# Kernel optimization log

Measured on AMD Instinct MI355X. Metric: run time of the kernel, lower is better.

Reference implementation:

```python
import jax, jax.numpy as jnp
import numpy as np

NEG_INF = -9e15
ALPHA = 0.2  # LeakyReLU negative slope


def setup_inputs() -> dict:
    key = jax.random.key(0)
    k1, k2, k3, k4 = jax.random.split(key, 4)
    N, F_in, F_out = 8192, 128, 64
    h = jax.random.normal(k1, (N, F_in), dtype=jnp.float32)
    adj = jax.random.randint(k2, (N, N), 0, 2, dtype=jnp.int32)
    W = jax.random.normal(k3, (F_in, F_out), dtype=jnp.float32) * (1.414 / np.sqrt(F_in))
    a = jax.random.normal(k4, (2 * F_out, 1), dtype=jnp.float32) * 0.1
    return {"h": h, "adj": adj, "W": W, "a": a}


def reference(h, adj, W, a):
    # Wh: [N, F_out]
    Wh = h @ W
    F_out = Wh.shape[1]
    # Decomposed additive score: cat([Wh_i, Wh_j]) @ a == Wh_i@a1 + Wh_j@a2.
    # Identical math to the original repeat/cat/mm, without the [N*N, 2F] blowup.
    s1 = Wh @ a[:F_out, 0]   # [N] source-side score
    s2 = Wh @ a[F_out:, 0]   # [N] target-side score
    e = jax.nn.leaky_relu(s1[:, None] + s2[None, :], negative_slope=ALPHA)  # [N, N]
    attention = jax.nn.softmax(jnp.where(adj > 0, e, NEG_INF), axis=1)
    # dropout is identity in eval mode
    h_prime = attention @ Wh  # [N, F_out]
    return (h_prime, attention)
```

## Files before the change

### kernel.cpp

```cpp
#include <hip/hip_runtime.h>

#define NN 8192
#define FIN 128
#define FOUT 64
#define NEGINF (-9e15f)
#define LALPHA 0.2f

typedef float f32x4 __attribute__((ext_vector_type(4)));
typedef short short8 __attribute__((ext_vector_type(8)));

__device__ __forceinline__ unsigned short f32_to_bf16(float x) {
  unsigned int u = __float_as_uint(x);
  u = (u + 0x7fffu + ((u >> 16) & 1u)) >> 16;
  return (unsigned short)u;
}
__device__ __forceinline__ float bf16_to_f32(unsigned short b) {
  return __uint_as_float(((unsigned int)b) << 16);
}

__global__ __launch_bounds__(256) void gat_prep(
    const float* __restrict__ h, const float* __restrict__ W,
    const float* __restrict__ a,
    float* __restrict__ s1g, float* __restrict__ s2g,
    unsigned short* __restrict__ whfh)
{
  __shared__ __align__(16) float Wl[FIN * FOUT];
  __shared__ __align__(16) float hl[16 * FIN];
  const int tid = threadIdx.x;
  const int i0 = blockIdx.x * 16;
  #pragma unroll
  for (int it = 0; it < 8; ++it) {
    int idx = (it * 256 + tid) * 4;
    *(f32x4*)&Wl[idx] = *(const f32x4*)&W[idx];
  }
  #pragma unroll
  for (int it = 0; it < 2; ++it) {
    int idx = (it * 256 + tid) * 4;
    *(f32x4*)&hl[idx] = *(const f32x4*)&h[(size_t)i0 * FIN + idx];
  }
  __syncthreads();
  const int r = tid >> 4;
  const int f0 = (tid & 15) * 4;
  f32x4 acc = {0.f, 0.f, 0.f, 0.f};
  #pragma unroll 8
  for (int k = 0; k < FIN; ++k) {
    float hv = hl[r * FIN + k];
    f32x4 wv = *(const f32x4*)&Wl[k * FOUT + f0];
    acc += hv * wv;
  }
  f32x4 a1v = *(const f32x4*)&a[f0];
  f32x4 a2v = *(const f32x4*)&a[FOUT + f0];
  float p1 = acc.x * a1v.x + acc.y * a1v.y + acc.z * a1v.z + acc.w * a1v.w;
  float p2 = acc.x * a2v.x + acc.y * a2v.y + acc.z * a2v.z + acc.w * a2v.w;
  #pragma unroll
  for (int d = 1; d < 16; d <<= 1) {
    p1 += __shfl_xor(p1, d, 16);
    p2 += __shfl_xor(p2, d, 16);
  }
  const int j = i0 + r;
  if ((tid & 15) == 0) { s1g[j] = p1; s2g[j] = p2; }
  const int kstep = j >> 5;
  const int lhi = (j >> 3) & 3;
  const int ein = j & 7;
  #pragma unroll
  for (int e = 0; e < 4; ++e) {
    int f = f0 + e;
    unsigned short hb = f32_to_bf16(acc[e]);
    int ln = lhi * 16 + (f & 15);
    whfh[(size_t)(kstep * 4 + (f >> 4)) * 512 + ln * 8 + ein] = hb;
  }
}

__global__ __launch_bounds__(256, 2) void gat_main(
    const int* __restrict__ adj,
    const float* __restrict__ s1g, const float* __restrict__ s2g,
    const unsigned short* __restrict__ whfh,
    float* __restrict__ outh, float* __restrict__ outa)
{
  __shared__ __align__(16) float s2l[NN];
  __shared__ __align__(16) unsigned int maskl[16][257];
  __shared__ float rowp[16][4];
  const int tid = threadIdx.x;
  const int lane = tid & 63;
  const int wv = tid >> 6;
  const int i0 = blockIdx.x * 16;

  #pragma unroll
  for (int it = 0; it < 8; ++it) {
    int idx = (it * 256 + tid) * 4;
    *(f32x4*)&s2l[idx] = *(const f32x4*)&s2g[idx];
  }
  __syncthreads();

  {
    const int rbase = wv * 4;
    const int* __restrict__ ar0 = adj + (size_t)(i0 + rbase + 0) * NN;
    const int* __restrict__ ar1 = adj + (size_t)(i0 + rbase + 1) * NN;
    const int* __restrict__ ar2 = adj + (size_t)(i0 + rbase + 2) * NN;
    const int* __restrict__ ar3 = adj + (size_t)(i0 + rbase + 3) * NN;
    float mx0 = -3.4e38f, mx1 = -3.4e38f, mx2 = -3.4e38f, mx3 = -3.4e38f;
    #pragma unroll 2
    for (int it = 0; it < 128; ++it) {
      int jj = it * 64 + lane;
      float sv = s2l[jj];
      int a0 = __builtin_nontemporal_load(&ar0[jj]);
      int a1 = __builtin_nontemporal_load(&ar1[jj]);
      int a2 = __builtin_nontemporal_load(&ar2[jj]);
      int a3 = __builtin_nontemporal_load(&ar3[jj]);
      unsigned long long b0 = __ballot(a0 > 0);
      unsigned long long b1 = __ballot(a1 > 0);
      unsigned long long b2 = __ballot(a2 > 0);
      unsigned long long b3 = __ballot(a3 > 0);
      mx0 = fmaxf(mx0, (a0 > 0) ? sv : -3.4e38f);
      mx1 = fmaxf(mx1, (a1 > 0) ? sv : -3.4e38f);
      mx2 = fmaxf(mx2, (a2 > 0) ? sv : -3.4e38f);
      mx3 = fmaxf(mx3, (a3 > 0) ? sv : -3.4e38f);
      if ((lane & 31) == 0) {
        int hi = lane >> 5;
        maskl[rbase + 0][it * 2 + hi] = (unsigned int)(b0 >> (hi * 32));
        maskl[rbase + 1][it * 2 + hi] = (unsigned int)(b1 >> (hi * 32));
        maskl[rbase + 2][it * 2 + hi] = (unsigned int)(b2 >> (hi * 32));
        maskl[rbase + 3][it * 2 + hi] = (unsigned int)(b3 >> (hi * 32));
      }
    }
    float mxs[4] = {mx0, mx1, mx2, mx3};
    #pragma unroll
    for (int rr = 0; rr < 4; ++rr) {
      float ms = mxs[rr];
      #pragma unroll
      for (int d = 1; d < 64; d <<= 1) ms = fmaxf(ms, __shfl_xor(ms, d));
      float s1v = s1g[i0 + rbase + rr];
      float z = s1v + ms;
      float m = (ms <= -3.3e38f) ? NEGINF : (z >= 0.f ? z : LALPHA * z);
      float ls = 0.f;
      for (int it = 0; it < 128; ++it) {
        int jj = it * 64 + lane;
        unsigned int wrd = maskl[rbase + rr][it * 2 + (lane >> 5)];
        float x = s1v + s2l[jj];
        x = (x >= 0.f) ? x : LALPHA * x;
        x = ((wrd >> (lane & 31)) & 1u) ? x : NEGINF;
        ls += __expf(x - m);
      }
      #pragma unroll
      for (int d = 1; d < 64; d <<= 1) ls += __shfl_xor(ls, d);
      if (lane == 0) {
        rowp[rbase + rr][0] = s1v;
        rowp[rbase + rr][1] = m;
        rowp[rbase + rr][2] = 1.f / ls;
      }
    }
  }
  __syncthreads();

  const int row = lane & 15;
  const int kg = lane >> 4;
  const float s1r = rowp[row][0];
  const float mr = rowp[row][1];
  const float rir = rowp[row][2];
  const int kbase = wv * 2048;
  f32x4 acc0 = {0,0,0,0}, acc1 = {0,0,0,0}, acc2 = {0,0,0,0}, acc3 = {0,0,0,0};
  float* __restrict__ orow = outa + (size_t)(i0 + row) * NN;
  const short8* __restrict__ bfrag = (const short8*)whfh;
  for (int step = 0; step < 64; ++step) {
    const int k0 = kbase + step * 32;
    const int jb = k0 + kg * 8;
    f32x4 sa = *(const f32x4*)&s2l[jb];
    f32x4 sb = *(const f32x4*)&s2l[jb + 4];
    unsigned int bits = maskl[row][k0 >> 5] >> (kg * 8);
    float s2v[8] = {sa.x, sa.y, sa.z, sa.w, sb.x, sb.y, sb.z, sb.w};
    float af[8];
    short8 AH, AL;
    #pragma unroll
    for (int e = 0; e < 8; ++e) {
      float x = s1r + s2v[e];
      x = (x >= 0.f) ? x : LALPHA * x;
      x = ((bits >> e) & 1u) ? x : NEGINF;
      float p = __expf(x - mr) * rir;
      af[e] = p;
      unsigned short hb = f32_to_bf16(p);
      AH[e] = (short)hb;
      AL[e] = (short)f32_to_bf16(p - bf16_to_f32(hb));
    }
    f32x4 st0 = {af[0], af[1], af[2], af[3]};
    f32x4 st1 = {af[4], af[5], af[6], af[7]};
    __builtin_nontemporal_store(st0, (f32x4*)&orow[jb]);
    __builtin_nontemporal_store(st1, (f32x4*)&orow[jb + 4]);
    size_t fb = (size_t)(k0 >> 5) * 256 + lane;
    short8 B0 = bfrag[fb];
    short8 B1 = bfrag[fb + 64];
    short8 B2 = bfrag[fb + 128];
    short8 B3 = bfrag[fb + 192];
    acc0 = __builtin_amdgcn_mfma_f32_16x16x32_bf16(AH, B0, acc0, 0, 0, 0);
    acc1 = __builtin_amdgcn_mfma_f32_16x16x32_bf16(AH, B1, acc1, 0, 0, 0);
    acc2 = __builtin_amdgcn_mfma_f32_16x16x32_bf16(AH, B2, acc2, 0, 0, 0);
    acc3 = __builtin_amdgcn_mfma_f32_16x16x32_bf16(AH, B3, acc3, 0, 0, 0);
    acc0 = __builtin_amdgcn_mfma_f32_16x16x32_bf16(AL, B0, acc0, 0, 0, 0);
    acc1 = __builtin_amdgcn_mfma_f32_16x16x32_bf16(AL, B1, acc1, 0, 0, 0);
    acc2 = __builtin_amdgcn_mfma_f32_16x16x32_bf16(AL, B2, acc2, 0, 0, 0);
    acc3 = __builtin_amdgcn_mfma_f32_16x16x32_bf16(AL, B3, acc3, 0, 0, 0);
  }
  __syncthreads();
  float* red = (float*)&maskl[0][0];
  {
    const int c15 = lane & 15;
    f32x4 av[4] = {acc0, acc1, acc2, acc3};
    #pragma unroll
    for (int nt = 0; nt < 4; ++nt) {
      #pragma unroll
      for (int rg = 0; rg < 4; ++rg) {
        red[wv * 1024 + (kg * 4 + rg) * 64 + nt * 16 + c15] = av[nt][rg];
      }
    }
  }
  __syncthreads();
  {
    int base = tid * 4;
    f32x4 r0 = *(f32x4*)&red[base];
    f32x4 r1 = *(f32x4*)&red[1024 + base];
    f32x4 r2 = *(f32x4*)&red[2048 + base];
    f32x4 r3 = *(f32x4*)&red[3072 + base];
    f32x4 s = r0 + r1 + r2 + r3;
    *(f32x4*)&outh[(size_t)i0 * FOUT + base] = s;
  }
}

extern "C" void kernel_launch(void* const* d_in, const int* in_sizes, int n_in,
                              void* d_out, int out_size, void* d_ws, size_t ws_size,
                              hipStream_t stream) {
  const float* h = (const float*)d_in[0];
  const int* adj = (const int*)d_in[1];
  const float* W = (const float*)d_in[2];
  const float* a = (const float*)d_in[3];
  float* outh = (float*)d_out;
  float* outa = outh + (size_t)NN * FOUT;
  char* ws = (char*)d_ws;
  float* s1g = (float*)ws;
  float* s2g = s1g + NN;
  unsigned short* whfh = (unsigned short*)(ws + 64 * 1024);
  gat_prep<<<512, 256, 0, stream>>>(h, W, a, s1g, s2g, whfh);
  gat_main<<<512, 256, 0, stream>>>(adj, s1g, s2g, whfh, outh, outa);
}
```

Measured before the change: 528.4 us.

## Split mask/softmax-stats pass into separate kernel and widen attention blocks

Moves the adjacency scan, row max and row sum into a new kernel that handles one row per wave across 2048 blocks. It stashes the bitmask in the first 1KB of each output attention row, and the attention kernel reloads it from there before overwriting. The attention/MFMA kernel now uses 512 threads (8 waves) with a two-stage LDS reduction. The aim is more parallelism in the adj-reading phase and higher occupancy in the compute phase, at the cost of an extra launch and a global round trip for the mask and stats.

```diff
diff --git a/kernel.cpp b/kernel.cpp
--- a/kernel.cpp
+++ b/kernel.cpp
@@ -7,6 +7,7 @@
 #define LALPHA 0.2f
 
 typedef float f32x4 __attribute__((ext_vector_type(4)));
+typedef float f32x2 __attribute__((ext_vector_type(2)));
 typedef short short8 __attribute__((ext_vector_type(8)));
 
 __device__ __forceinline__ unsigned short f32_to_bf16(float x) {
@@ -71,84 +72,86 @@
   }
 }
 
-__global__ __launch_bounds__(256, 2) void gat_main(
+__global__ __launch_bounds__(256, 4) void gat_mask(
     const int* __restrict__ adj,
     const float* __restrict__ s1g, const float* __restrict__ s2g,
+    float* __restrict__ outa,
+    float* __restrict__ mrow, float* __restrict__ rlrow)
+{
+  __shared__ __align__(16) float s2l[NN];
+  __shared__ unsigned long long mw[4][128];
+  const int tid = threadIdx.x;
+  const int lane = tid & 63;
+  const int wv = tid >> 6;
+  const int row = blockIdx.x * 4 + wv;
+  #pragma unroll
+  for (int it = 0; it < 8; ++it) {
+    int idx = (it * 256 + tid) * 4;
+    *(f32x4*)&s2l[idx] = *(const f32x4*)&s2g[idx];
+  }
+  __syncthreads();
+  const int* __restrict__ ar = adj + (size_t)row * NN;
+  float mx = -3.4e38f;
+  #pragma unroll 4
+  for (int it = 0; it < 128; ++it) {
+    int jj = it * 64 + lane;
+    int av = __builtin_nontemporal_load(&ar[jj]);
+    unsigned long long b = __ballot(av > 0);
+    mx = fmaxf(mx, (av > 0) ? s2l[jj] : -3.4e38f);
+    if (lane == 0) mw[wv][it] = b;
+  }
+  #pragma unroll
+  for (int d = 1; d < 64; d <<= 1) mx = fmaxf(mx, __shfl_xor(mx, d));
+  const float s1v = s1g[row];
+  const float z = s1v + mx;
+  const float m = (mx <= -3.3e38f) ? NEGINF : fmaxf(z, LALPHA * z);
+  float ls = 0.f;
+  for (int it = 0; it < 128; ++it) {
+    int jj = it * 64 + lane;
+    unsigned long long b = mw[wv][it];
+    float x = s1v + s2l[jj];
+    x = fmaxf(x, LALPHA * x);
+    x = ((b >> lane) & 1ull) ? x : NEGINF;
+    ls += __expf(x - m);
+  }
+  #pragma unroll
+  for (int d = 1; d < 64; d <<= 1) ls += __shfl_xor(ls, d);
+  if (lane == 0) { mrow[row] = m; rlrow[row] = 1.f / ls; }
+  unsigned long long* mrowg = (unsigned long long*)(outa + (size_t)row * NN);
+  mrowg[lane] = mw[wv][lane];
+  mrowg[lane + 64] = mw[wv][lane + 64];
+}
+
+__global__ __launch_bounds__(512, 4) void gat_attn(
+    const float* __restrict__ s1g, const float* __restrict__ s2g,
+    const float* __restrict__ mrow, const float* __restrict__ rlrow,
     const unsigned short* __restrict__ whfh,
     float* __restrict__ outh, float* __restrict__ outa)
 {
   __shared__ __align__(16) float s2l[NN];
-  __shared__ __align__(16) unsigned int maskl[16][257];
-  __shared__ float rowp[16][4];
+  __shared__ unsigned int maskl[16][258];
+  __shared__ __align__(16) float red[4][1024];
+  __shared__ float rowp[16][3];
   const int tid = threadIdx.x;
   const int lane = tid & 63;
   const int wv = tid >> 6;
   const int i0 = blockIdx.x * 16;
 
   #pragma unroll
-  for (int it = 0; it < 8; ++it) {
-    int idx = (it * 256 + tid) * 4;
+  for (int it = 0; it < 4; ++it) {
+    int idx = (it * 512 + tid) * 4;
     *(f32x4*)&s2l[idx] = *(const f32x4*)&s2g[idx];
   }
-  __syncthreads();
-
-  {
-    const int rbase = wv * 4;
-    const int* __restrict__ ar0 = adj + (size_t)(i0 + rbase + 0) * NN;
-    const int* __restrict__ ar1 = adj + (size_t)(i0 + rbase + 1) * NN;
-    const int* __restrict__ ar2 = adj + (size_t)(i0 + rbase + 2) * NN;
-    const int* __restrict__ ar3 = adj + (size_t)(i0 + rbase + 3) * NN;
-    float mx0 = -3.4e38f, mx1 = -3.4e38f, mx2 = -3.4e38f, mx3 = -3.4e38f;
-    #pragma unroll 2
-    for (int it = 0; it < 128; ++it) {
-      int jj = it * 64 + lane;
-      float sv = s2l[jj];
-      int a0 = __builtin_nontemporal_load(&ar0[jj]);
-      int a1 = __builtin_nontemporal_load(&ar1[jj]);
-      int a2 = __builtin_nontemporal_load(&ar2[jj]);
-      int a3 = __builtin_nontemporal_load(&ar3[jj]);
-      unsigned long long b0 = __ballot(a0 > 0);
-      unsigned long long b1 = __ballot(a1 > 0);
-      unsigned long long b2 = __ballot(a2 > 0);
-      unsigned long long b3 = __ballot(a3 > 0);
-      mx0 = fmaxf(mx0, (a0 > 0) ? sv : -3.4e38f);
-      mx1 = fmaxf(mx1, (a1 > 0) ? sv : -3.4e38f);
-      mx2 = fmaxf(mx2, (a2 > 0) ? sv : -3.4e38f);
-      mx3 = fmaxf(mx3, (a3 > 0) ? sv : -3.4e38f);
-      if ((lane & 31) == 0) {
-        int hi = lane >> 5;
-        maskl[rbase + 0][it * 2 + hi] = (unsigned int)(b0 >> (hi * 32));
-        maskl[rbase + 1][it * 2 + hi] = (unsigned int)(b1 >> (hi * 32));
-        maskl[rbase + 2][it * 2 + hi] = (unsigned int)(b2 >> (hi * 32));
-        maskl[rbase + 3][it * 2 + hi] = (unsigned int)(b3 >> (hi * 32));
-      }
-    }
-    float mxs[4] = {mx0, mx1, mx2, mx3};
-    #pragma unroll
-    for (int rr = 0; rr < 4; ++rr) {
-      float ms = mxs[rr];
-      #pragma unroll
-      for (int d = 1; d < 64; d <<= 1) ms = fmaxf(ms, __shfl_xor(ms, d));
-      float s1v = s1g[i0 + rbase + rr];
-      float z = s1v + ms;
-      float m = (ms <= -3.3e38f) ? NEGINF : (z >= 0.f ? z : LALPHA * z);
-      float ls = 0.f;
-      for (int it = 0; it < 128; ++it) {
-        int jj = it * 64 + lane;
-        unsigned int wrd = maskl[rbase + rr][it * 2 + (lane >> 5)];
-        float x = s1v + s2l[jj];
-        x = (x >= 0.f) ? x : LALPHA * x;
-        x = ((wrd >> (lane & 31)) & 1u) ? x : NEGINF;
-        ls += __expf(x - m);
-      }
-      #pragma unroll
-      for (int d = 1; d < 64; d <<= 1) ls += __shfl_xor(ls, d);
-      if (lane == 0) {
-        rowp[rbase + rr][0] = s1v;
-        rowp[rbase + rr][1] = m;
-        rowp[rbase + rr][2] = 1.f / ls;
-      }
-    }
+  #pragma unroll
+  for (int i = 0; i < 8; ++i) {
+    int idx = i * 512 + tid;
+    int r = idx >> 8, w = idx & 255;
+    maskl[r][w] = ((const unsigned int*)(outa + (size_t)(i0 + r) * NN))[w];
+  }
+  if (tid < 16) {
+    rowp[tid][0] = s1g[i0 + tid];
+    rowp[tid][1] = mrow[i0 + tid];
+    rowp[tid][2] = rlrow[i0 + tid];
   }
   __syncthreads();
 
@@ -157,11 +160,11 @@
   const float s1r = rowp[row][0];
   const float mr = rowp[row][1];
   const float rir = rowp[row][2];
-  const int kbase = wv * 2048;
+  const int kbase = wv * 1024;
   f32x4 acc0 = {0,0,0,0}, acc1 = {0,0,0,0}, acc2 = {0,0,0,0}, acc3 = {0,0,0,0};
   float* __restrict__ orow = outa + (size_t)(i0 + row) * NN;
   const short8* __restrict__ bfrag = (const short8*)whfh;
-  for (int step = 0; step < 64; ++step) {
+  for (int step = 0; step < 32; ++step) {
     const int k0 = kbase + step * 32;
     const int jb = k0 + kg * 8;
     f32x4 sa = *(const f32x4*)&s2l[jb];
@@ -173,7 +176,7 @@
     #pragma unroll
     for (int e = 0; e < 8; ++e) {
       float x = s1r + s2v[e];
-      x = (x >= 0.f) ? x : LALPHA * x;
+      x = fmaxf(x, LALPHA * x);
       x = ((bits >> e) & 1u) ? x : NEGINF;
       float p = __expf(x - mr) * rir;
       af[e] = p;
@@ -199,28 +202,33 @@
     acc2 = __builtin_amdgcn_mfma_f32_16x16x32_bf16(AL, B2, acc2, 0, 0, 0);
     acc3 = __builtin_amdgcn_mfma_f32_16x16x32_bf16(AL, B3, acc3, 0, 0, 0);
   }
-  __syncthreads();
-  float* red = (float*)&maskl[0][0];
+  const int c15 = lane & 15;
+  f32x4 av[4] = {acc0, acc1, acc2, acc3};
+  float* myred = &red[wv & 3][0];
+  if (wv < 4) {
+    #pragma unroll
+    for (int nt = 0; nt < 4; ++nt)
+      #pragma unroll
+      for (int rg = 0; rg < 4; ++rg)
+        myred[(kg * 4 + rg) * 64 + nt * 16 + c15] = av[nt][rg];
+  }
+  __syncthreads();
+  if (wv >= 4) {
+    #pragma unroll
+    for (int nt = 0; nt < 4; ++nt)
+      #pragma unroll
+      for (int rg = 0; rg < 4; ++rg)
+        myred[(kg * 4 + rg) * 64 + nt * 16 + c15] += av[nt][rg];
+  }
+  __syncthreads();
   {
-    const int c15 = lane & 15;
-    f32x4 av[4] = {acc0, acc1, acc2, acc3};
-    #pragma unroll
-    for (int nt = 0; nt < 4; ++nt) {
-      #pragma unroll
-      for (int rg = 0; rg < 4; ++rg) {
-        red[wv * 1024 + (kg * 4 + rg) * 64 + nt * 16 + c15] = av[nt][rg];
-      }
-    }
-  }
-  __syncthreads();
-  {
-    int base = tid * 4;
-    f32x4 r0 = *(f32x4*)&red[base];
-    f32x4 r1 = *(f32x4*)&red[1024 + base];
-    f32x4 r2 = *(f32x4*)&red[2048 + base];
-    f32x4 r3 = *(f32x4*)&red[3072 + base];
-    f32x4 s = r0 + r1 + r2 + r3;
-    *(f32x4*)&outh[(size_t)i0 * FOUT + base] = s;
+    int base = tid * 2;
+    f32x2 r0 = *(f32x2*)&red[0][base];
+    f32x2 r1 = *(f32x2*)&red[1][base];
+    f32x2 r2 = *(f32x2*)&red[2][base];
+    f32x2 r3 = *(f32x2*)&red[3][base];
+    f32x2 s = r0 + r1 + r2 + r3;
+    *(f32x2*)&outh[(size_t)i0 * FOUT + base] = s;
   }
 }
 
@@ -236,7 +244,10 @@
   char* ws = (char*)d_ws;
   float* s1g = (float*)ws;
   float* s2g = s1g + NN;
-  unsigned short* whfh = (unsigned short*)(ws + 64 * 1024);
+  float* mrowv = s2g + NN;
+  float* rlrowv = mrowv + NN;
+  unsigned short* whfh = (unsigned short*)(ws + 128 * 1024);
   gat_prep<<<512, 256, 0, stream>>>(h, W, a, s1g, s2g, whfh);
-  gat_main<<<512, 256, 0, stream>>>(adj, s1g, s2g, whfh, outh, outa);
-}
+  gat_mask<<<2048, 256, 0, stream>>>(adj, s1g, s2g, outa, mrowv, rlrowv);
+  gat_attn<<<512, 512, 0, stream>>>(s1g, s2g, mrowv, rlrowv, whfh, outh, outa);
+}
```

Measured after the change: 584.0 us. +10.5%, slower.
